# Performance work log

Hardware: AMD Instinct MI355X
Metric: run time of the kernel (lower is better)

The kernel has to match this reference:

```python
import jax, jax.numpy as jnp
import numpy as np

# physical constants from init_kwargs
N_ACT = 10.0                      # adaptive_activation_n (same for all layers)
MU1, MU2 = 1.0, 10.0
SIGMA = 24.5
G = 0.98
RHO1, RHO2 = 100.0, 1000.0
U_REF, L_REF = 1.0, 0.5
RHO_REF = RHO2
EPS = 2.220446049250313e-16       # np.finfo(float).eps used in abs_interface_grad
ONE_WE = SIGMA / (RHO_REF * U_REF ** 2 * L_REF)
ONE_FR = G * L_REF / U_REF ** 2
RE_DEN = RHO_REF * U_REF * L_REF


def setup_inputs() -> dict:
    key = jax.random.key(0)
    ks = jax.random.split(key, 8)
    N, H, NL = 32768, 250, 7

    def glorot(k, shape):
        fan_in, fan_out = shape[-2], shape[-1]
        s = jnp.sqrt(2.0 / (fan_in + fan_out)).astype(jnp.float32)
        return jax.random.normal(k, shape, dtype=jnp.float32) * s

    return {
        "x": jax.random.normal(ks[0], (N, 1), dtype=jnp.float32),
        "y": jax.random.normal(ks[1], (N, 1), dtype=jnp.float32),
        "t": jax.random.uniform(ks[2], (N, 1), dtype=jnp.float32),
        "W_in": glorot(ks[3], (3, H)),
        "b_in": jnp.zeros((H,), jnp.float32),
        "W_h": glorot(ks[4], (NL - 1, H, H)),
        "b_h": jnp.zeros((NL - 1, H), jnp.float32),
        "W_out": glorot(ks[5], (H, 4)),   # 4 heads: u, v, p, a
        "b_out": jnp.zeros((4,), jnp.float32),
        "act_coeff": jnp.full((NL,), 0.1, jnp.float32),  # adaptive activation coeffs
    }


def _mlp(pt, W_in, b_in, W_h, b_h, W_out, b_out, act_coeff):
    # pt: (3,) -> (4,) outputs [u, v, p=exp(z), a=sigmoid(z)]
    h = jnp.tanh(N_ACT * act_coeff[0] * (pt @ W_in + b_in))
    for i in range(W_h.shape[0]):  # structural loop over 6 hidden layers
        h = jnp.tanh(N_ACT * act_coeff[i + 1] * (h @ W_h[i] + b_h[i]))
    z = h @ W_out + b_out
    return jnp.stack([z[0], z[1], jnp.exp(z[2]), jax.nn.sigmoid(z[3])])


def _pde_residuals(x, y, t, W_in, b_in, W_h, b_h, W_out, b_out, act_coeff):
    pts = jnp.concatenate([x, y, t], axis=1)  # (N, 3)
    f = lambda p: _mlp(p, W_in, b_in, W_h, b_h, W_out, b_out, act_coeff)
    vals = jax.vmap(f)(pts)                              # (N, 4)
    jac = jax.vmap(jax.jacfwd(f))(pts)                   # (N, 4, 3)
    hess = jax.vmap(jax.jacfwd(jax.jacfwd(f)))(pts)      # (N, 4, 3, 3)

    u, v, a = vals[:, 0], vals[:, 1], vals[:, 3]
    u_x, u_y, u_t = jac[:, 0, 0], jac[:, 0, 1], jac[:, 0, 2]
    v_x, v_y, v_t = jac[:, 1, 0], jac[:, 1, 1], jac[:, 1, 2]
    p_x, p_y = jac[:, 2, 0], jac[:, 2, 1]
    a_x, a_y, a_t = jac[:, 3, 0], jac[:, 3, 1], jac[:, 3, 2]
    u_xx, u_yy = hess[:, 0, 0, 0], hess[:, 0, 1, 1]
    v_xx, v_yy = hess[:, 1, 0, 0], hess[:, 1, 1, 1]
    a_xx, a_yy, a_xy = hess[:, 3, 0, 0], hess[:, 3, 1, 1], hess[:, 3, 0, 1]

    mu = MU2 + (MU1 - MU2) * a
    mu_x = (MU1 - MU2) * a_x
    mu_y = (MU1 - MU2) * a_y
    rho = RHO2 + (RHO1 - RHO2) * a

    g = jnp.sqrt(a_x ** 2 + a_y ** 2 + EPS)
    curvature = -((a_xx + a_yy) / g
                  - (a_x ** 2 * a_xx + a_y ** 2 * a_yy + 2.0 * a_x * a_y * a_xy) / (g ** 3))

    one_Re = mu / RE_DEN
    one_Re_x = mu_x / RE_DEN
    one_Re_y = mu_y / RE_DEN

    PDE_m = u_x + v_y
    PDE_a = a_t + u * a_x + v * a_y
    PDE_u = ((u_t + u * u_x + v * u_y) * rho / RHO_REF + p_x
             - ONE_WE * curvature * a_x - one_Re * (u_xx + u_yy)
             - 2.0 * one_Re_x * u_x - one_Re_y * (u_y + v_x))
    PDE_v = ((v_t + u * v_x + v * v_y) * rho / RHO_REF + p_y
             - ONE_WE * curvature * a_y - one_Re * (v_xx + v_yy)
             - rho / RHO_REF * ONE_FR
             - 2.0 * one_Re_y * v_y - one_Re_x * (u_y + v_x))
    return jnp.stack([PDE_m, PDE_u, PDE_v, PDE_a], axis=1)  # (N, 4)


def reference(x, y, t, W_in, b_in, W_h, b_h, W_out, b_out, act_coeff):
    r = _pde_residuals(x, y, t, W_in, b_in, W_h, b_h, W_out, b_out, act_coeff)
    # match PDE_caller's tuple of (N,1) residuals
    return (r[:, 0:1], r[:, 1:2], r[:, 2:3], r[:, 3:4])
```

## Files before the change

### kernel.cpp

```cpp
#include <hip/hip_runtime.h>
#include <math.h>
#include <stdint.h>

#define HP 256
#define PTS 16
#define ROWS 128
#define PSTR 264
#define NLAYER 6
#define WT_ELEMS (6*256*256)

typedef _Float16 half8 __attribute__((ext_vector_type(8)));
typedef float  float16v __attribute__((ext_vector_type(16)));

#define C_WI 0
#define C_BI 768
#define C_BH 1024
#define C_WO 2560
#define C_TOT 3584

__device__ __forceinline__ float fast_tanh(float x) {
    float e = __expf(2.0f * x);
    return 1.0f - __fdividef(2.0f, e + 1.0f);
}

__device__ __forceinline__ float16v zero16() {
    float16v z;
    #pragma unroll
    for (int i = 0; i < 16; ++i) z[i] = 0.0f;
    return z;
}

__device__ __forceinline__ int arow(int P, int c) {
    return 32*(P >> 2) + 16*((P >> 1) & 1) + 4*(P & 1) + 8*(c >> 2) + (c & 3);
}

#define MFMA16(A,B,Cc) __builtin_amdgcn_mfma_f32_32x32x16_f16((A),(B),(Cc),0,0,0)

__global__ void prep_kernel(const float* __restrict__ W_in, const float* __restrict__ b_in,
                            const float* __restrict__ W_h,  const float* __restrict__ b_h,
                            const float* __restrict__ W_out, void* __restrict__ wsv)
{
    _Float16* wt = (_Float16*)wsv;
    float* cf = (float*)((char*)wsv + (size_t)WT_ELEMS * 2);

    int i0 = blockIdx.x * blockDim.x + threadIdx.x;
    int stride = gridDim.x * blockDim.x;
    for (int i = i0; i < WT_ELEMS; i += stride) {
        int j    = i & 7;
        int lane = (i >> 3) & 63;
        int st   = (i >> 9) & 7;
        int s    = (i >> 12) & 15;
        int L    = i >> 16;
        int lo5 = lane & 31, hi5 = lane >> 5;
        int n = 32*st + lo5;
        int k = 16*s + 8*hi5 + j;
        wt[i] = (_Float16)((n < 250 && k < 250) ? W_h[(L*250 + k)*250 + n] : 0.0f);
    }
    for (int i = i0; i < C_TOT; i += stride) {
        float v = 0.0f;
        if (i < C_BI) { int r = i >> 8, j = i & 255; if (j < 250) v = W_in[r*250 + j]; }
        else if (i < C_BH) { int j = i - C_BI; if (j < 250) v = b_in[j]; }
        else if (i < C_WO) { int idx = i - C_BH; int l = idx >> 8, j = idx & 255; if (j < 250) v = b_h[l*250 + j]; }
        else { int idx = i - C_WO; int k = idx >> 2, o = idx & 3; if (k < 250) v = W_out[k*4 + o]; }
        cf[i] = v;
    }
}

__launch_bounds__(512, 4)
__global__ void pinn_mfma(const float* __restrict__ xg, const float* __restrict__ yg,
                          const float* __restrict__ tg, const void* __restrict__ wsv,
                          const float* __restrict__ b_out, const float* __restrict__ act,
                          float* __restrict__ out, int N)
{
    __shared__ _Float16 Ah[ROWS * PSTR];
    __shared__ float zo[PTS][28];

    const _Float16* __restrict__ wt = (const _Float16*)wsv;
    const float* __restrict__ cf = (const float*)((const char*)wsv + (size_t)WT_ELEMS * 2);

    const int tid  = threadIdx.x;
    const int lane = tid & 63;
    const int w    = tid >> 6;
    const int lo5  = lane & 31;
    const int hi5  = lane >> 5;
    const int n0   = 32*w + lo5;

    {
        int j   = tid & 255;
        int hf  = tid >> 8;
        float wi0 = cf[C_WI + j], wi1 = cf[C_WI + 256 + j], wi2 = cf[C_WI + 512 + j];
        float biv = cf[C_BI + j];
        float c0 = 10.0f * act[0];
        #pragma unroll
        for (int p8 = 0; p8 < 8; ++p8) {
            int p  = 8*hf + p8;
            int gp = blockIdx.x * PTS + p;
            gp = gp < N ? gp : N - 1;
            float px = xg[gp], py = yg[gp], pt = tg[gp];
            float z = px*wi0 + py*wi1 + pt*wi2 + biv;
            float y = fast_tanh(c0 * z);
            float s = 1.0f - y*y;
            float cs = c0 * s;
            float m2 = -2.0f * c0 * cs * y;
            float o[8];
            o[0] = y;           o[1] = cs*wi0;      o[2] = cs*wi1;      o[3] = cs*wi2;
            o[4] = m2*wi0*wi0;  o[5] = m2*wi1*wi1;  o[6] = m2*wi0*wi1;  o[7] = 0.0f;
            #pragma unroll
            for (int c = 0; c < 8; ++c)
                Ah[arow(p, c)*PSTR + j] = (_Float16)o[c];
        }
    }

    for (int L = 0; L < NLAYER; ++L) {
        float cc = 10.0f * act[L + 1];
        const _Float16* __restrict__ ph = wt + ((size_t)L << 16) + ((size_t)w << 9)
                                             + (size_t)lane * 8;

        half8 Bq[4];
        #pragma unroll
        for (int i = 0; i < 4; ++i)
            Bq[i] = *(const half8*)(ph + 4096*i);

        float16v m[4];
        #pragma unroll
        for (int rt = 0; rt < 4; ++rt) m[rt] = zero16();

        __syncthreads();

        const int abase = lo5 * PSTR + 8*hi5;
        half8 a0[4], a1[4];
        #pragma unroll
        for (int rt = 0; rt < 4; ++rt) {
            a0[rt] = *(const half8*)&Ah[abase + 32*rt*PSTR];
            a1[rt] = *(const half8*)&Ah[abase + 32*rt*PSTR + 16];
        }

        #pragma unroll
        for (int s = 0; s < 16; ++s) {
            half8 b = Bq[s & 3];
            if (s < 12)
                Bq[s & 3] = *(const half8*)(ph + 4096*(s + 4));
            half8 cur[4];
            #pragma unroll
            for (int rt = 0; rt < 4; ++rt) { cur[rt] = a0[rt]; a0[rt] = a1[rt]; }
            if (s < 14) {
                #pragma unroll
                for (int rt = 0; rt < 4; ++rt)
                    a1[rt] = *(const half8*)&Ah[abase + 32*rt*PSTR + 16*(s + 2)];
            }
            #pragma unroll
            for (int rt = 0; rt < 4; ++rt)
                m[rt] = MFMA16(cur[rt], b, m[rt]);
        }

        __syncthreads();

        float bb = cf[C_BH + (L << 8) + n0];

        #pragma unroll
        for (int rt = 0; rt < 4; ++rt) {
            float16v mv = m[rt];
            #pragma unroll
            for (int pp = 0; pp < 2; ++pp) {
                float z   = mv[8*pp+0] + bb;
                float zx  = mv[8*pp+1];
                float zy  = mv[8*pp+2];
                float zt  = mv[8*pp+3];
                float zxx = mv[8*pp+4];
                float zyy = mv[8*pp+5];
                float zxy = mv[8*pp+6];
                float y   = fast_tanh(cc * z);
                float sh  = 1.0f - y*y;
                float cs  = cc * sh;
                float m2c = -2.0f * cc * cs * y;
                int r0 = (32*rt + 16*pp + 4*hi5) * PSTR + n0;
                Ah[r0 + 0*PSTR] = (_Float16)y;
                Ah[r0 + 1*PSTR] = (_Float16)(cs*zx);
                Ah[r0 + 2*PSTR] = (_Float16)(cs*zy);
                Ah[r0 + 3*PSTR] = (_Float16)(cs*zt);
                int r1 = r0 + 8*PSTR;
                Ah[r1 + 0*PSTR] = (_Float16)(cs*zxx + m2c*zx*zx);
                Ah[r1 + 1*PSTR] = (_Float16)(cs*zyy + m2c*zy*zy);
                Ah[r1 + 2*PSTR] = (_Float16)(cs*zxy + m2c*zx*zy);
                Ah[r1 + 3*PSTR] = (_Float16)0.0f;
            }
        }
    }

    __syncthreads();
    if (tid < PTS * 28) {
        int p = tid / 28, idx = tid % 28;
        int c = idx >> 2, o = idx & 3;
        const _Float16* rh = &Ah[arow(p, c) * PSTR];
        float s = 0.0f;
        for (int k = 0; k < HP; ++k)
            s += (float)rh[k] * cf[C_WO + 4*k + o];
        zo[p][idx] = s;
    }
    __syncthreads();

    if (tid < PTS) {
        int gp = blockIdx.x * PTS + tid;
        if (gp < N) {
            float zc[7][4];
            #pragma unroll
            for (int c = 0; c < 7; ++c)
                #pragma unroll
                for (int o = 0; o < 4; ++o)
                    zc[c][o] = zo[tid][c*4 + o] + (c == 0 ? b_out[o] : 0.0f);

            float u  = zc[0][0], vv = zc[0][1];
            float u_x = zc[1][0], u_y = zc[2][0], u_t = zc[3][0];
            float u_xx = zc[4][0], u_yy = zc[5][0];
            float v_x = zc[1][1], v_y = zc[2][1], v_t = zc[3][1];
            float v_xx = zc[4][1], v_yy = zc[5][1];

            float ep  = expf(zc[0][2]);
            float p_x = ep * zc[1][2], p_y = ep * zc[2][2];

            float a   = 1.0f / (1.0f + expf(-zc[0][3]));
            float sp  = a * (1.0f - a);
            float spp = sp * (1.0f - 2.0f*a);
            float z1a = zc[1][3], z2a = zc[2][3];
            float a_x = sp * z1a, a_y = sp * z2a, a_t = sp * zc[3][3];
            float a_xx = spp*z1a*z1a + sp*zc[4][3];
            float a_yy = spp*z2a*z2a + sp*zc[5][3];
            float a_xy = spp*z1a*z2a + sp*zc[6][3];

            float mu_x = -9.0f*a_x, mu_y = -9.0f*a_y;
            float mu   = 10.0f - 9.0f*a;
            float rr   = 1.0f - 0.9f*a;
            float g  = sqrtf(a_x*a_x + a_y*a_y + 2.220446049250313e-16f);
            float g3 = g*g*g;
            float curv = -((a_xx + a_yy)/g
                         - (a_x*a_x*a_xx + a_y*a_y*a_yy + 2.0f*a_x*a_y*a_xy)/g3);
            float one_Re   = mu   * 0.002f;
            float one_Re_x = mu_x * 0.002f;
            float one_Re_y = mu_y * 0.002f;

            float PDE_m = u_x + v_y;
            float PDE_a = a_t + u*a_x + vv*a_y;
            float PDE_u = (u_t + u*u_x + vv*u_y)*rr + p_x - 0.049f*curv*a_x
                        - one_Re*(u_xx + u_yy) - 2.0f*one_Re_x*u_x - one_Re_y*(u_y + v_x);
            float PDE_v = (v_t + u*v_x + vv*v_y)*rr + p_y - 0.049f*curv*a_y
                        - one_Re*(v_xx + v_yy) - rr*0.49f
                        - 2.0f*one_Re_y*v_y - one_Re_x*(u_y + v_x);

            out[0*N + gp] = PDE_m;
            out[1*N + gp] = PDE_u;
            out[2*N + gp] = PDE_v;
            out[3*N + gp] = PDE_a;
        }
    }
}

extern "C" void kernel_launch(void* const* d_in, const int* in_sizes, int n_in,
                              void* d_out, int out_size, void* d_ws, size_t ws_size,
                              hipStream_t stream)
{
    const float* x     = (const float*)d_in[0];
    const float* y     = (const float*)d_in[1];
    const float* t     = (const float*)d_in[2];
    const float* W_in  = (const float*)d_in[3];
    const float* b_in  = (const float*)d_in[4];
    const float* W_h   = (const float*)d_in[5];
    const float* b_h   = (const float*)d_in[6];
    const float* W_out = (const float*)d_in[7];
    const float* b_out = (const float*)d_in[8];
    const float* act   = (const float*)d_in[9];
    float* out = (float*)d_out;
    int N = in_sizes[0];

    hipLaunchKernelGGL(prep_kernel, dim3(512), dim3(256), 0, stream,
                       W_in, b_in, W_h, b_h, W_out, d_ws);
    int nb = (N + PTS - 1) / PTS;
    hipLaunchKernelGGL(pinn_mfma, dim3(nb), dim3(512), 0, stream,
                       x, y, t, d_ws, b_out, act, out, N);
}
```

Measured before the change: 313.7 us.

## Tile-transpose weight prep, vectorize output head with fdot2, stagger block start

The weight-swizzle prep kernel now transposes 64x64 tiles through shared memory, so global reads are coalesced and the swizzled fp16 layout is written as 8-wide vectors. This replaces the scattered strided gathers. W_out is also stored as a transposed fp16 copy, so the output-head dot product uses 8-wide vector loads and packed fdot2, at slightly lower accumulation precision. Odd blocks of the main kernel sleep briefly at start, apparently to desynchronize phases between co-resident blocks, which adds a small fixed delay.

```diff
diff --git a/kernel.cpp b/kernel.cpp
--- a/kernel.cpp
+++ b/kernel.cpp
@@ -8,8 +8,10 @@
 #define PSTR 264
 #define NLAYER 6
 #define WT_ELEMS (6*256*256)
+#define PREP_TILES 96
 
 typedef _Float16 half8 __attribute__((ext_vector_type(8)));
+typedef _Float16 half2v __attribute__((ext_vector_type(2)));
 typedef float  float16v __attribute__((ext_vector_type(16)));
 
 #define C_WI 0
@@ -42,27 +44,59 @@
 {
     _Float16* wt = (_Float16*)wsv;
     float* cf = (float*)((char*)wsv + (size_t)WT_ELEMS * 2);
-
-    int i0 = blockIdx.x * blockDim.x + threadIdx.x;
-    int stride = gridDim.x * blockDim.x;
-    for (int i = i0; i < WT_ELEMS; i += stride) {
-        int j    = i & 7;
-        int lane = (i >> 3) & 63;
-        int st   = (i >> 9) & 7;
-        int s    = (i >> 12) & 15;
-        int L    = i >> 16;
-        int lo5 = lane & 31, hi5 = lane >> 5;
-        int n = 32*st + lo5;
-        int k = 16*s + 8*hi5 + j;
-        wt[i] = (_Float16)((n < 250 && k < 250) ? W_h[(L*250 + k)*250 + n] : 0.0f);
-    }
-    for (int i = i0; i < C_TOT; i += stride) {
-        float v = 0.0f;
-        if (i < C_BI) { int r = i >> 8, j = i & 255; if (j < 250) v = W_in[r*250 + j]; }
-        else if (i < C_BH) { int j = i - C_BI; if (j < 250) v = b_in[j]; }
-        else if (i < C_WO) { int idx = i - C_BH; int l = idx >> 8, j = idx & 255; if (j < 250) v = b_h[l*250 + j]; }
-        else { int idx = i - C_WO; int k = idx >> 2, o = idx & 3; if (k < 250) v = W_out[k*4 + o]; }
-        cf[i] = v;
+    _Float16* cfh = (_Float16*)(cf + C_TOT);
+
+    const int tid = threadIdx.x;
+    const int bid = blockIdx.x;
+
+    if (bid < PREP_TILES) {
+        __shared__ _Float16 tile[64 * 65];
+        int l  = bid / 16;
+        int ka = (bid % 16) >> 2;
+        int na = bid & 3;
+        int k0 = 64 * ka, n0 = 64 * na;
+        #pragma unroll
+        for (int pass = 0; pass < 16; ++pass) {
+            int idx = pass * 256 + tid;
+            int kl = idx >> 6, nl = idx & 63;
+            int k = k0 + kl, n = n0 + nl;
+            float v = (k < 250 && n < 250) ? W_h[(l*250 + k)*250 + n] : 0.0f;
+            tile[kl * 65 + nl] = (_Float16)v;
+        }
+        __syncthreads();
+        #pragma unroll
+        for (int b = 0; b < 2; ++b) {
+            int slot = tid * 2 + b;
+            int lo5  = slot & 31;
+            int st_l = (slot >> 5) & 1;
+            int hi5  = (slot >> 6) & 1;
+            int s_l  = slot >> 7;
+            int nl = st_l * 32 + lo5;
+            half8 hv;
+            #pragma unroll
+            for (int j = 0; j < 8; ++j)
+                hv[j] = tile[(s_l * 16 + hi5 * 8 + j) * 65 + nl];
+            int s    = ka * 4 + s_l;
+            int st   = na * 2 + st_l;
+            int lane = hi5 * 32 + lo5;
+            size_t dst = ((size_t)l << 16) | (s << 12) | (st << 9) | (lane << 3);
+            *(half8*)(wt + dst) = hv;
+        }
+    } else {
+        int i0 = (bid - PREP_TILES) * blockDim.x + tid;
+        int stride = 8 * blockDim.x;
+        for (int i = i0; i < C_TOT; i += stride) {
+            float v = 0.0f;
+            if (i < C_BI) { int r = i >> 8, j = i & 255; if (j < 250) v = W_in[r*250 + j]; }
+            else if (i < C_BH) { int j = i - C_BI; if (j < 250) v = b_in[j]; }
+            else if (i < C_WO) { int idx = i - C_BH; int l = idx >> 8, j = idx & 255; if (j < 250) v = b_h[l*250 + j]; }
+            else { int idx = i - C_WO; int k = idx >> 2, o = idx & 3; if (k < 250) v = W_out[k*4 + o]; }
+            cf[i] = v;
+        }
+        for (int i = i0; i < 1024; i += stride) {
+            int o = i >> 8, k = i & 255;
+            cfh[i] = (_Float16)(k < 250 ? W_out[k*4 + o] : 0.0f);
+        }
     }
 }
 
@@ -77,6 +111,14 @@
 
     const _Float16* __restrict__ wt = (const _Float16*)wsv;
     const float* __restrict__ cf = (const float*)((const char*)wsv + (size_t)WT_ELEMS * 2);
+    const _Float16* __restrict__ cfh = (const _Float16*)(cf + C_TOT);
+
+    if (blockIdx.x & 1) {
+        __builtin_amdgcn_s_sleep(32);
+        __builtin_amdgcn_s_sleep(32);
+        __builtin_amdgcn_s_sleep(32);
+        __builtin_amdgcn_s_sleep(32);
+    }
 
     const int tid  = threadIdx.x;
     const int lane = tid & 63;
@@ -192,9 +234,23 @@
         int p = tid / 28, idx = tid % 28;
         int c = idx >> 2, o = idx & 3;
         const _Float16* rh = &Ah[arow(p, c) * PSTR];
+        const _Float16* wo = cfh + (o << 8);
         float s = 0.0f;
-        for (int k = 0; k < HP; ++k)
-            s += (float)rh[k] * cf[C_WO + 4*k + o];
+        for (int kq = 0; kq < HP/8; ++kq) {
+            half8 h  = *(const half8*)(rh + 8*kq);
+            half8 ww = *(const half8*)(wo + 8*kq);
+#if __has_builtin(__builtin_amdgcn_fdot2)
+            #pragma unroll
+            for (int j = 0; j < 4; ++j) {
+                half2v ha = { h[2*j], h[2*j+1] };
+                half2v wa = { ww[2*j], ww[2*j+1] };
+                s = __builtin_amdgcn_fdot2(ha, wa, s, false);
+            }
+#else
+            #pragma unroll
+            for (int j = 0; j < 8; ++j) s += (float)h[j] * (float)ww[j];
+#endif
+        }
         zo[p][idx] = s;
     }
     __syncthreads();
@@ -271,7 +327,7 @@
     float* out = (float*)d_out;
     int N = in_sizes[0];
 
-    hipLaunchKernelGGL(prep_kernel, dim3(512), dim3(256), 0, stream,
+    hipLaunchKernelGGL(prep_kernel, dim3(PREP_TILES + 8), dim3(256), 0, stream,
                        W_in, b_in, W_h, b_h, W_out, d_ws);
     int nb = (N + PTS - 1) / PTS;
     hipLaunchKernelGGL(pinn_mfma, dim3(nb), dim3(512), 0, stream,
```

Measured after the change: 335.8 us. 1.07x slower.
